# Optimization experiments

Measured on AMD Instinct MI355X. Metric: run time of the kernel, lower is better.

## Reference

```python
import jax, jax.numpy as jnp
import numpy as np

N_QUBITS = 13
DEPTH = 4
DIM = 2 ** N_QUBITS
PI = 3.141592653589793

# qubit 0 = most significant bit of the basis-state index
_idx = np.arange(DIM)
BITS = np.stack([(_idx >> (N_QUBITS - 1 - q)) & 1 for q in range(N_QUBITS)], axis=1)  # (DIM, n)
SIGNS = jnp.asarray(1.0 - 2.0 * BITS, dtype=jnp.float32)                               # Z eigenvalues, (DIM, n)
PARITY = jnp.asarray((-1.0) ** BITS.sum(axis=1), dtype=jnp.float32)                    # <Z^{(x)n}> diagonal, (DIM,)
# CZ entangling chain (q, q+1): diagonal (-1)^{sum_q b_q b_{q+1}}
ENT = jnp.asarray((-1.0) ** (BITS[:, :-1] * BITS[:, 1:]).sum(axis=1), dtype=jnp.float32)


def fwht(psi):
    """Normalized fast Walsh-Hadamard transform (H on every qubit), psi: (B, DIM) complex."""
    B = psi.shape[0]
    for q in range(N_QUBITS):
        psi = psi.reshape(B, 2 ** q, 2, -1)
        psi = jnp.stack([psi[:, :, 0] + psi[:, :, 1], psi[:, :, 0] - psi[:, :, 1]], axis=2)
    return psi.reshape(B, DIM) * (2.0 ** (-N_QUBITS / 2))


def feature_map_state(x):
    """Havlicek ZZ feature map: psi = D(x) H^n D(x) H^n |0...0>.
    Diagonal phase per basis state b: sum_j x_j s_j(b) + sum_{j<k} (pi-x_j)(pi-x_k) s_j(b) s_k(b)."""
    a = PI - x                                              # (B, n)
    u = x @ SIGNS.T                                         # (B, DIM)
    v = a @ SIGNS.T                                         # (B, DIM)
    phi = u + 0.5 * (v * v - jnp.sum(a * a, axis=1, keepdims=True))  # pair term via (sum)^2 trick
    d = jnp.exp(1j * phi)                                   # complex64 diagonal
    psi = jnp.full((x.shape[0], DIM), DIM ** -0.5, dtype=jnp.complex64)  # H^n |0>
    psi = fwht(d * psi)
    return d * psi


def _apply_1q(psi, U, q):
    """Apply 2x2 complex gate U to qubit q (bit-sliced)."""
    B = psi.shape[0]
    psi = psi.reshape(B, 2 ** q, 2, -1)
    a0, a1 = psi[:, :, 0], psi[:, :, 1]
    out = jnp.stack([U[0, 0] * a0 + U[0, 1] * a1, U[1, 0] * a0 + U[1, 1] * a1], axis=2)
    return out.reshape(B, DIM)


def variational_apply(psi, theta):
    """(DEPTH+1) layers of per-qubit Rz(b)Ry(a), CZ-chain entanglers between layers."""
    th = theta.reshape(DEPTH + 1, N_QUBITS, 2)
    for l in range(DEPTH + 1):
        if l > 0:
            psi = psi * ENT
        for q in range(N_QUBITS):
            ca = jnp.cos(0.5 * th[l, q, 0])
            sa = jnp.sin(0.5 * th[l, q, 0])
            em = jnp.exp(-0.5j * th[l, q, 1])
            ep = jnp.exp(0.5j * th[l, q, 1])
            U = jnp.stack([jnp.stack([em * ca, -em * sa]), jnp.stack([ep * sa, ep * ca])])
            psi = _apply_1q(psi, U, q)
    return psi


def setup_inputs() -> dict:
    key = jax.random.key(0)
    k1, k2 = jax.random.split(key)
    x = jax.random.normal(k1, (512, N_QUBITS), dtype=jnp.float32)
    theta = 0.1 * jax.random.normal(k2, ((DEPTH + 1) * N_QUBITS * 2,), dtype=jnp.float32)
    bias = jnp.zeros((1,), dtype=jnp.float32)
    return {"x": x, "theta": theta, "bias": bias}


def reference(x, theta, bias):
    psi = feature_map_state(x)
    psi = variational_apply(psi, theta)
    prob = psi.real ** 2 + psi.imag ** 2              # (B, DIM)
    logit = prob @ PARITY + bias[0]                   # (B,)
    return jnp.stack([-logit, logit], axis=1)         # two-class logits
```

## Files before the change

### kernel.cpp

```cpp
#include <hip/hip_runtime.h>
#include <hip/hip_fp16.h>

#define NQ   13
#define DIM  8192
#define PI_F 3.14159265358979323846f
#define NT   256
#define NAMP 32

__device__ __forceinline__ int lslot(int i) { return i + 4 * (i >> 5); }
#define NSLOT (DIM + 4 * (DIM >> 5))

__device__ __forceinline__ int base0(int t) { return 36 * t; }
__device__ __forceinline__ int base2(int t, int g) { return 1152 * g + 4 * t + 4 * (t >> 3); }
__device__ __forceinline__ int slot1(int t, int j) { return 1152 * (t >> 5) + 36 * j + (t & 31); }

union F4H { float4 f; __half2 h[4]; };

__device__ __forceinline__ void rsincos(float x, float* s, float* c) {
  const float INV2PI = 0.15915494309189535f;
  const float TWOPI  = 6.283185307179586f;
  float r = x * INV2PI;
  r -= rintf(r);
  float ang = r * TWOPI;
  *s = __sinf(ang);
  *c = __cosf(ang);
}

__device__ __forceinline__ void waveFence() {
  __builtin_amdgcn_wave_barrier();
  __threadfence_block();
  __builtin_amdgcn_wave_barrier();
}

__device__ __forceinline__ float2 f2fma(float s, float2 a, float2 b) {
  return make_float2(fmaf(s, a.x, b.x), fmaf(s, a.y, b.y));
}
__device__ __forceinline__ float2 f2add(float2 a, float2 b) {
  return make_float2(a.x + b.x, a.y + b.y);
}
__device__ __forceinline__ float2 f2sub(float2 a, float2 b) {
  return make_float2(a.x - b.x, a.y - b.y);
}
__device__ __forceinline__ float2 cphase(float2 v, float cs, float sn) {
  return make_float2(fmaf(cs, v.x, -sn * v.y), fmaf(cs, v.y, sn * v.x));
}
__device__ __forceinline__ float2 cmul(float2 a, float2 b) {
  return make_float2(fmaf(a.x, b.x, -a.y * b.y), fmaf(a.x, b.y, a.y * b.x));
}

template<int PAT>
__device__ __forceinline__ int ampIndex(int t, int j) {
  if constexpr (PAT == 0) return (t << 5) | j;
  else if constexpr (PAT == 1) return ((t >> 5) << 10) | (j << 5) | (t & 31);
  else return ((j >> 2) << 10) | (t << 2) | (j & 3);
}

template<int PAT>
__device__ __forceinline__ void buildTree(const float* __restrict__ w, float bias,
                                          int t, float* s) {
  float base = bias;
  if constexpr (PAT == 0) {
    #pragma unroll
    for (int k = 0; k < 8; k++) base += ((t >> k) & 1) ? w[5 + k] : 0.0f;
  } else {
    #pragma unroll
    for (int k = 0; k < 8; k++) base += ((t >> k) & 1) ? w[2 + k] : 0.0f;
  }
  constexpr int P[5] = { 0, 1,
                         (PAT == 0) ? 2 : 10,
                         (PAT == 0) ? 3 : 11,
                         (PAT == 0) ? 4 : 12 };
  s[0] = base;
  #pragma unroll
  for (int k = 0; k < 5; k++) {
    float wp = w[P[k]];
    #pragma unroll
    for (int m = 0; m < (1 << k); m++) s[m | (1 << k)] = s[m] + wp;
  }
}

__device__ __forceinline__ void loadA0f(const __half2* __restrict__ sAmp, int t, float2* amp) {
  const __half2* p = sAmp + base0(t);
  #pragma unroll
  for (int k = 0; k < 8; k++) {
    F4H u; u.f = *reinterpret_cast<const float4*>(p + 4 * k);
    #pragma unroll
    for (int c = 0; c < 4; c++) amp[4 * k + c] = __half22float2(u.h[c]);
  }
}
__device__ __forceinline__ void storeA0f(__half2* __restrict__ sAmp, int t, const float2* amp) {
  __half2* p = sAmp + base0(t);
  #pragma unroll
  for (int k = 0; k < 8; k++) {
    F4H u;
    #pragma unroll
    for (int c = 0; c < 4; c++) u.h[c] = __float22half2_rn(amp[4 * k + c]);
    *reinterpret_cast<float4*>(p + 4 * k) = u.f;
  }
}
__device__ __forceinline__ void loadA2f(const __half2* __restrict__ sAmp, int t, float2* amp) {
  #pragma unroll
  for (int g = 0; g < 8; g++) {
    F4H u; u.f = *reinterpret_cast<const float4*>(sAmp + base2(t, g));
    #pragma unroll
    for (int c = 0; c < 4; c++) amp[4 * g + c] = __half22float2(u.h[c]);
  }
}
__device__ __forceinline__ void storeA2f(__half2* __restrict__ sAmp, int t, const float2* amp) {
  #pragma unroll
  for (int g = 0; g < 8; g++) {
    F4H u;
    #pragma unroll
    for (int c = 0; c < 4; c++) u.h[c] = __float22half2_rn(amp[4 * g + c]);
    *reinterpret_cast<float4*>(sAmp + base2(t, g)) = u.f;
  }
}

__device__ __forceinline__ void loadA1h(const __half2* __restrict__ sAmp, int t, __half2* amp) {
  #pragma unroll
  for (int j = 0; j < NAMP; j++) amp[j] = sAmp[slot1(t, j)];
}
__device__ __forceinline__ void storeA1h(__half2* __restrict__ sAmp, int t, const __half2* amp) {
  #pragma unroll
  for (int j = 0; j < NAMP; j++) sAmp[slot1(t, j)] = amp[j];
}
__device__ __forceinline__ void loadA2h(const __half2* __restrict__ sAmp, int t, __half2* amp) {
  #pragma unroll
  for (int g = 0; g < 8; g++) {
    F4H u; u.f = *reinterpret_cast<const float4*>(sAmp + base2(t, g));
    #pragma unroll
    for (int c = 0; c < 4; c++) amp[4 * g + c] = u.h[c];
  }
}
__device__ __forceinline__ void storeA2h(__half2* __restrict__ sAmp, int t, const __half2* amp) {
  #pragma unroll
  for (int g = 0; g < 8; g++) {
    F4H u;
    #pragma unroll
    for (int c = 0; c < 4; c++) u.h[c] = amp[4 * g + c];
    *reinterpret_cast<float4*>(sAmp + base2(t, g)) = u.f;
  }
}

template<int KB>
__device__ __forceinline__ void fwht_bit(float2* amp) {
  #pragma unroll
  for (int j = 0; j < NAMP; j++) if (!(j & (1 << KB))) {
    int j1 = j | (1 << KB);
    float2 a0 = amp[j], a1 = amp[j1];
    amp[j]  = f2add(a0, a1);
    amp[j1] = f2sub(a0, a1);
  }
}
template<int KB>
__device__ __forceinline__ void applyRy(float2* amp, float ta, float sa) {
  #pragma unroll
  for (int j = 0; j < NAMP; j++) if (!(j & (1 << KB))) {
    int j1 = j | (1 << KB);
    amp[j]  = f2fma(-ta, amp[j1], amp[j]);
    amp[j1] = f2fma( sa, amp[j],  amp[j1]);
    amp[j]  = f2fma(-ta, amp[j1], amp[j]);
  }
}

template<int KB>
__device__ __forceinline__ void fwht_bitH(__half2* amp) {
  #pragma unroll
  for (int j = 0; j < NAMP; j++) if (!(j & (1 << KB))) {
    int j1 = j | (1 << KB);
    __half2 a0 = amp[j], a1 = amp[j1];
    amp[j]  = __hadd2(a0, a1);
    amp[j1] = __hsub2(a0, a1);
  }
}
template<int KB>
__device__ __forceinline__ void applyRyH(__half2* amp, __half2 nta, __half2 sa) {
  #pragma unroll
  for (int j = 0; j < NAMP; j++) if (!(j & (1 << KB))) {
    int j1 = j | (1 << KB);
    amp[j]  = __hfma2(nta, amp[j1], amp[j]);
    amp[j1] = __hfma2(sa,  amp[j],  amp[j1]);
    amp[j]  = __hfma2(nta, amp[j1], amp[j]);
  }
}

template<int PAT, bool INIT>
__device__ __forceinline__ void featureDiag(float2* amp,
                                            const float* __restrict__ wX,
                                            const float* __restrict__ wA,
                                            const float* __restrict__ cons, int t) {
  float u[NAMP], v[NAMP];
  buildTree<PAT>(wX, cons[0], t, u);
  buildTree<PAT>(wA, cons[1], t, v);
  float A2 = cons[2];
  #pragma unroll
  for (int j = 0; j < NAMP; j++) {
    float phi = u[j] + 0.5f * (v[j] * v[j] - A2);
    float sn, cs; rsincos(phi, &sn, &cs);
    if constexpr (INIT) amp[j] = make_float2(cs, sn);
    else                amp[j] = cphase(amp[j], cs, sn);
  }
}

__device__ __forceinline__ void applyDiagPT(float2* amp,
                                            const float* __restrict__ wb,
                                            const float* __restrict__ eR,
                                            const float* __restrict__ eI,
                                            float bias, int t) {
  float base = bias;
  #pragma unroll
  for (int k = 0; k < 8; k++) base += ((t >> k) & 1) ? wb[5 + k] : 0.0f;
  float2 c[16];
  { float sn, cs; rsincos(base, &sn, &cs); c[0] = make_float2(cs, sn); }
  #pragma unroll
  for (int k = 0; k < 4; k++) {
    float2 e = make_float2(eR[k], eI[k]);
    #pragma unroll
    for (int m = 0; m < (1 << k); m++) c[m | (1 << k)] = cmul(c[m], e);
  }
  #pragma unroll
  for (int j = 0; j < 16; j++) {
    int i = ampIndex<0>(t, j);
    float sgn = (__popc(i & (i >> 1)) & 1) ? -1.0f : 1.0f;
    amp[j] = cphase(amp[j], c[j].x * sgn, c[j].y * sgn);
  }
  float2 e4 = make_float2(eR[4], eI[4]);
  #pragma unroll
  for (int j = 16; j < 32; j++) {
    int i = ampIndex<0>(t, j);
    float sgn = (__popc(i & (i >> 1)) & 1) ? -1.0f : 1.0f;
    float2 cc = cmul(c[j - 16], e4);
    amp[j] = cphase(amp[j], cc.x * sgn, cc.y * sgn);
  }
}

__global__ __launch_bounds__(NT, 1) void qc_kernel(
    const float* __restrict__ xin,
    const float* __restrict__ thin,
    const float* __restrict__ bin,
    float* __restrict__ out) {
  __shared__ alignas(16) __half2 sAmp[NSLOT];
  __shared__ float gTA[65], gSA[65];
  __shared__ __half2 hNTA[65], hSA[65];
  __shared__ float gBbit[65];
  __shared__ float eBr[65], eBi[65];
  __shared__ float wX[13], wA[13];
  __shared__ float cons[8];
  __shared__ float red[NT / 64];

  const int t = threadIdx.x;
  const int b = blockIdx.x;

  if (t < NQ) {
    float xq = xin[b * NQ + t];
    float aq = PI_F - xq;
    wX[12 - t] = -2.0f * xq;
    wA[12 - t] = -2.0f * aq;
  }
  if (t < 65) {
    float av = thin[2 * t];
    float bv = thin[2 * t + 1];
    float ca = cosf(0.5f * av);
    float sa = sinf(0.5f * av);
    float ta = sa / (1.0f + ca);
    gTA[t] = ta;
    gSA[t] = sa;
    hNTA[t] = __float2half2_rn(-ta);
    hSA[t]  = __float2half2_rn(sa);
    int l = t / NQ, q = t % NQ;
    int s = l * NQ + (12 - q);
    gBbit[s] = bv;
    eBr[s] = cosf(bv);
    eBi[s] = sinf(bv);
  }
  __syncthreads();
  if (t == 0) {
    float X = 0.f, A = 0.f, A2 = 0.f;
    for (int p = 0; p < NQ; p++) {
      float xq = -0.5f * wX[p], aq = -0.5f * wA[p];
      X += xq; A += aq; A2 += aq * aq;
    }
    cons[0] = X; cons[1] = A; cons[2] = A2;
    for (int l = 0; l < 5; l++) {
      float s = 0.f;
      for (int p = 0; p < NQ; p++) s += gBbit[l * NQ + p];
      cons[3 + l] = -0.5f * s;
    }
  }
  __syncthreads();

  {
    float2 amp[NAMP];
    featureDiag<0, true>(amp, wX, wA, cons, t);
    fwht_bit<0>(amp); fwht_bit<1>(amp); fwht_bit<2>(amp);
    fwht_bit<3>(amp); fwht_bit<4>(amp);
    storeA0f(sAmp, t, amp);
  }
  waveFence();

  {
    __half2 amp[NAMP];
    loadA1h(sAmp, t, amp);
    fwht_bitH<0>(amp); fwht_bitH<1>(amp); fwht_bitH<2>(amp);
    fwht_bitH<3>(amp); fwht_bitH<4>(amp);
    storeA1h(sAmp, t, amp);
  }
  __syncthreads();

  {
    float2 amp[NAMP];
    loadA2f(sAmp, t, amp);
    fwht_bit<2>(amp); fwht_bit<3>(amp); fwht_bit<4>(amp);
    featureDiag<2, false>(amp, wX, wA, cons, t);
    storeA2f(sAmp, t, amp);
  }
  __syncthreads();

  float acc = 0.0f;
  for (int l = 0; l < 5; l++) {
    const int g = l * NQ;
    {
      float2 amp[NAMP];
      loadA0f(sAmp, t, amp);
      if (l > 0) applyDiagPT(amp, gBbit + (l - 1) * NQ, eBr + (l - 1) * NQ,
                             eBi + (l - 1) * NQ, cons[3 + (l - 1)], t);
      applyRy<0>(amp, gTA[g + 12], gSA[g + 12]);
      applyRy<1>(amp, gTA[g + 11], gSA[g + 11]);
      applyRy<2>(amp, gTA[g + 10], gSA[g + 10]);
      applyRy<3>(amp, gTA[g + 9],  gSA[g + 9]);
      applyRy<4>(amp, gTA[g + 8],  gSA[g + 8]);
      storeA0f(sAmp, t, amp);
    }
    waveFence();
    {
      __half2 amp[NAMP];
      loadA1h(sAmp, t, amp);
      applyRyH<0>(amp, hNTA[g + 7], hSA[g + 7]);
      applyRyH<1>(amp, hNTA[g + 6], hSA[g + 6]);
      applyRyH<2>(amp, hNTA[g + 5], hSA[g + 5]);
      applyRyH<3>(amp, hNTA[g + 4], hSA[g + 4]);
      applyRyH<4>(amp, hNTA[g + 3], hSA[g + 3]);
      storeA1h(sAmp, t, amp);
    }
    __syncthreads();
    {
      __half2 amp[NAMP];
      loadA2h(sAmp, t, amp);
      applyRyH<2>(amp, hNTA[g + 2], hSA[g + 2]);
      applyRyH<3>(amp, hNTA[g + 1], hSA[g + 1]);
      applyRyH<4>(amp, hNTA[g + 0], hSA[g + 0]);
      if (l < 4) {
        storeA2h(sAmp, t, amp);
      } else {
        #pragma unroll
        for (int j = 0; j < NAMP; j++) {
          int i = ampIndex<2>(t, j);
          float2 a = __half22float2(amp[j]);
          float p2 = fmaf(a.x, a.x, a.y * a.y);
          acc += (__popc(i) & 1) ? -p2 : p2;
        }
      }
    }
    if (l < 4) __syncthreads();
  }

  #pragma unroll
  for (int off = 32; off > 0; off >>= 1) acc += __shfl_down(acc, off, 64);
  if ((t & 63) == 0) red[t >> 6] = acc;
  __syncthreads();
  if (t == 0) {
    float total = red[0] + red[1] + red[2] + red[3];
    float logit = total * (1.0f / 67108864.0f) + bin[0];
    out[b * 2 + 0] = -logit;
    out[b * 2 + 1] = logit;
  }
}

extern "C" void kernel_launch(void* const* d_in, const int* in_sizes, int n_in,
                              void* d_out, int out_size, void* d_ws, size_t ws_size,
                              hipStream_t stream) {
  const float* x  = (const float*)d_in[0];
  const float* th = (const float*)d_in[1];
  const float* bi = (const float*)d_in[2];
  float* out = (float*)d_out;
  int B = in_sizes[0] / NQ;
  qc_kernel<<<B, NT, 0, stream>>>(x, th, bi, out);
}
```

Measured before the change: 91.52 us.

## Regroup qubit stages so each layer needs fewer shared-memory passes and barriers

Restructures the per-layer gate schedule: the entangling diagonal and the Ry gates on qubits 0-2 and 11-12 move into the layout-2 pass, and that pass is merged with the previous layer's tail. Layer 0's gates for those qubits are folded into the feature-map pass. The goal is to drop one full load/store pass over shared memory per layer. The trade-off is that the layout-0 pass becomes a half-precision pass, and the layout-2 pass now does the float diagonal, which needs a new bit mapping.

```diff
diff --git a/kernel.cpp b/kernel.cpp
--- a/kernel.cpp
+++ b/kernel.cpp
@@ -116,6 +116,25 @@
   }
 }
 
+__device__ __forceinline__ void loadA0h(const __half2* __restrict__ sAmp, int t, __half2* amp) {
+  const __half2* p = sAmp + base0(t);
+  #pragma unroll
+  for (int k = 0; k < 8; k++) {
+    F4H u; u.f = *reinterpret_cast<const float4*>(p + 4 * k);
+    #pragma unroll
+    for (int c = 0; c < 4; c++) amp[4 * k + c] = u.h[c];
+  }
+}
+__device__ __forceinline__ void storeA0h(__half2* __restrict__ sAmp, int t, const __half2* amp) {
+  __half2* p = sAmp + base0(t);
+  #pragma unroll
+  for (int k = 0; k < 8; k++) {
+    F4H u;
+    #pragma unroll
+    for (int c = 0; c < 4; c++) u.h[c] = amp[4 * k + c];
+    *reinterpret_cast<float4*>(p + 4 * k) = u.f;
+  }
+}
 __device__ __forceinline__ void loadA1h(const __half2* __restrict__ sAmp, int t, __half2* amp) {
   #pragma unroll
   for (int j = 0; j < NAMP; j++) amp[j] = sAmp[slot1(t, j)];
@@ -123,23 +142,6 @@
 __device__ __forceinline__ void storeA1h(__half2* __restrict__ sAmp, int t, const __half2* amp) {
   #pragma unroll
   for (int j = 0; j < NAMP; j++) sAmp[slot1(t, j)] = amp[j];
-}
-__device__ __forceinline__ void loadA2h(const __half2* __restrict__ sAmp, int t, __half2* amp) {
-  #pragma unroll
-  for (int g = 0; g < 8; g++) {
-    F4H u; u.f = *reinterpret_cast<const float4*>(sAmp + base2(t, g));
-    #pragma unroll
-    for (int c = 0; c < 4; c++) amp[4 * g + c] = u.h[c];
-  }
-}
-__device__ __forceinline__ void storeA2h(__half2* __restrict__ sAmp, int t, const __half2* amp) {
-  #pragma unroll
-  for (int g = 0; g < 8; g++) {
-    F4H u;
-    #pragma unroll
-    for (int c = 0; c < 4; c++) u.h[c] = amp[4 * g + c];
-    *reinterpret_cast<float4*>(sAmp + base2(t, g)) = u.f;
-  }
 }
 
 template<int KB>
@@ -202,32 +204,33 @@
   }
 }
 
-__device__ __forceinline__ void applyDiagPT(float2* amp,
-                                            const float* __restrict__ wb,
-                                            const float* __restrict__ eR,
-                                            const float* __restrict__ eI,
-                                            float bias, int t) {
+__device__ __forceinline__ void applyDiagPT2(float2* amp,
+                                             const float* __restrict__ wb,
+                                             const float* __restrict__ eR,
+                                             const float* __restrict__ eI,
+                                             float bias, int t) {
   float base = bias;
   #pragma unroll
-  for (int k = 0; k < 8; k++) base += ((t >> k) & 1) ? wb[5 + k] : 0.0f;
+  for (int k = 0; k < 8; k++) base += ((t >> k) & 1) ? wb[2 + k] : 0.0f;
   float2 c[16];
   { float sn, cs; rsincos(base, &sn, &cs); c[0] = make_float2(cs, sn); }
+  constexpr int EB[4] = {0, 1, 10, 11};
   #pragma unroll
   for (int k = 0; k < 4; k++) {
-    float2 e = make_float2(eR[k], eI[k]);
+    float2 e = make_float2(eR[EB[k]], eI[EB[k]]);
     #pragma unroll
     for (int m = 0; m < (1 << k); m++) c[m | (1 << k)] = cmul(c[m], e);
   }
   #pragma unroll
   for (int j = 0; j < 16; j++) {
-    int i = ampIndex<0>(t, j);
+    int i = ampIndex<2>(t, j);
     float sgn = (__popc(i & (i >> 1)) & 1) ? -1.0f : 1.0f;
     amp[j] = cphase(amp[j], c[j].x * sgn, c[j].y * sgn);
   }
-  float2 e4 = make_float2(eR[4], eI[4]);
+  float2 e4 = make_float2(eR[12], eI[12]);
   #pragma unroll
   for (int j = 16; j < 32; j++) {
-    int i = ampIndex<0>(t, j);
+    int i = ampIndex<2>(t, j);
     float sgn = (__popc(i & (i >> 1)) & 1) ? -1.0f : 1.0f;
     float2 cc = cmul(c[j - 16], e4);
     amp[j] = cphase(amp[j], cc.x * sgn, cc.y * sgn);
@@ -312,6 +315,11 @@
     loadA2f(sAmp, t, amp);
     fwht_bit<2>(amp); fwht_bit<3>(amp); fwht_bit<4>(amp);
     featureDiag<2, false>(amp, wX, wA, cons, t);
+    applyRy<0>(amp, gTA[12], gSA[12]);
+    applyRy<1>(amp, gTA[11], gSA[11]);
+    applyRy<2>(amp, gTA[2],  gSA[2]);
+    applyRy<3>(amp, gTA[1],  gSA[1]);
+    applyRy<4>(amp, gTA[0],  gSA[0]);
     storeA2f(sAmp, t, amp);
   }
   __syncthreads();
@@ -320,16 +328,12 @@
   for (int l = 0; l < 5; l++) {
     const int g = l * NQ;
     {
-      float2 amp[NAMP];
-      loadA0f(sAmp, t, amp);
-      if (l > 0) applyDiagPT(amp, gBbit + (l - 1) * NQ, eBr + (l - 1) * NQ,
-                             eBi + (l - 1) * NQ, cons[3 + (l - 1)], t);
-      applyRy<0>(amp, gTA[g + 12], gSA[g + 12]);
-      applyRy<1>(amp, gTA[g + 11], gSA[g + 11]);
-      applyRy<2>(amp, gTA[g + 10], gSA[g + 10]);
-      applyRy<3>(amp, gTA[g + 9],  gSA[g + 9]);
-      applyRy<4>(amp, gTA[g + 8],  gSA[g + 8]);
-      storeA0f(sAmp, t, amp);
+      __half2 amp[NAMP];
+      loadA0h(sAmp, t, amp);
+      applyRyH<2>(amp, hNTA[g + 10], hSA[g + 10]);
+      applyRyH<3>(amp, hNTA[g + 9],  hSA[g + 9]);
+      applyRyH<4>(amp, hNTA[g + 8],  hSA[g + 8]);
+      storeA0h(sAmp, t, amp);
     }
     waveFence();
     {
@@ -340,28 +344,33 @@
       applyRyH<2>(amp, hNTA[g + 5], hSA[g + 5]);
       applyRyH<3>(amp, hNTA[g + 4], hSA[g + 4]);
       applyRyH<4>(amp, hNTA[g + 3], hSA[g + 3]);
-      storeA1h(sAmp, t, amp);
-    }
-    __syncthreads();
-    {
-      __half2 amp[NAMP];
-      loadA2h(sAmp, t, amp);
-      applyRyH<2>(amp, hNTA[g + 2], hSA[g + 2]);
-      applyRyH<3>(amp, hNTA[g + 1], hSA[g + 1]);
-      applyRyH<4>(amp, hNTA[g + 0], hSA[g + 0]);
       if (l < 4) {
-        storeA2h(sAmp, t, amp);
+        storeA1h(sAmp, t, amp);
       } else {
         #pragma unroll
         for (int j = 0; j < NAMP; j++) {
-          int i = ampIndex<2>(t, j);
+          int i = ampIndex<1>(t, j);
           float2 a = __half22float2(amp[j]);
           float p2 = fmaf(a.x, a.x, a.y * a.y);
           acc += (__popc(i) & 1) ? -p2 : p2;
         }
       }
     }
-    if (l < 4) __syncthreads();
+    if (l < 4) {
+      __syncthreads();
+      const int g1 = (l + 1) * NQ;
+      float2 amp[NAMP];
+      loadA2f(sAmp, t, amp);
+      applyDiagPT2(amp, gBbit + l * NQ, eBr + l * NQ, eBi + l * NQ,
+                   cons[3 + l], t);
+      applyRy<0>(amp, gTA[g1 + 12], gSA[g1 + 12]);
+      applyRy<1>(amp, gTA[g1 + 11], gSA[g1 + 11]);
+      applyRy<2>(amp, gTA[g1 + 2],  gSA[g1 + 2]);
+      applyRy<3>(amp, gTA[g1 + 1],  gSA[g1 + 1]);
+      applyRy<4>(amp, gTA[g1 + 0],  gSA[g1 + 0]);
+      storeA2f(sAmp, t, amp);
+      __syncthreads();
+    }
   }
 
   #pragma unroll
```

After: 89.23 us, median of 2. -2.5%, faster.
